# Optimization experiments

Hardware: AMD Instinct MI355X
Metric: run time of the kernel (lower is better)

## Reference

```python
import jax, jax.numpy as jnp
import numpy as np
from jax import lax

T_OBS = 16; N = 4096; V = 8; IN = 2; DYN = 64; ENC = 64; K = 2
SELF = 32; SOCD = 64; C31 = 16; DEC = 128; PRED = 25; OUT = 5; GH = 13; GW = 3
SOC_EMB = ((GH - 4 + 1) // 2) * C31  # 80


def leaky(v):
    return jnp.where(v >= 0, v, 0.1 * v)


def gru(xs, Wih, Whh, bih, bhh):
    # xs: [T, B, D]; PyTorch GRU cell math. Returns (h_T [B,H], all h [T,B,H]).
    H = Whh.shape[1]
    gis = xs @ Wih.T + bih  # precompute input contributions [T,B,3H]

    def step(h, gi):
        gh = h @ Whh.T + bhh
        ir, iz, inn = jnp.split(gi, 3, axis=-1)
        hr, hz, hn = jnp.split(gh, 3, axis=-1)
        r = jax.nn.sigmoid(ir + hr)
        z = jax.nn.sigmoid(iz + hz)
        n = jnp.tanh(inn + r * hn)
        h = (1.0 - z) * n + z * h
        return h, h

    h0 = jnp.zeros((xs.shape[1], H), xs.dtype)
    hT, hs = lax.scan(step, h0, gis)
    return hT, hs


def conv2d(xn, w, b):
    y = lax.conv_general_dilated(xn, w, (1, 1), 'VALID',
                                 dimension_numbers=('NCHW', 'OIHW', 'NCHW'))
    return y + b[None, :, None, None]


def setup_inputs() -> dict:
    key = jax.random.key(0)
    ks = jax.random.split(key, 24)
    x = jax.random.normal(ks[0], (T_OBS, N, IN), dtype=jnp.float32)
    ngbrs = jax.random.normal(ks[1], (T_OBS, N * V, IN), dtype=jnp.float32)
    # per-sample normalized spatial kernels [N, K, V, V]
    graphs = jax.random.uniform(ks[2], (N, K, V, V), dtype=jnp.float32) / V
    # masks: exactly V occupied grid cells per agent (full feature vector True)
    rng = np.random.default_rng(0)
    sel = np.argsort(rng.random((N, GW * GH)), axis=1)[:, :V]
    cell = np.zeros((N, GW * GH), dtype=bool)
    np.put_along_axis(cell, sel, True, axis=1)
    masks = jnp.asarray(np.broadcast_to(cell.reshape(N, GW, GH, 1), (N, GW, GH, ENC)))
    ngbrs_idx = jnp.arange(N + 1, dtype=jnp.int32) * V
    s = 0.05

    def w(k, shape):
        return jax.random.normal(k, shape, dtype=jnp.float32) * s

    params = dict(
        dyn_W=w(ks[3], (DYN, IN)), dyn_b=w(ks[4], (DYN,)),
        enc_Wih=w(ks[5], (3 * ENC, DYN)), enc_Whh=w(ks[6], (3 * ENC, ENC)),
        enc_bih=w(ks[7], (3 * ENC,)), enc_bhh=w(ks[8], (3 * ENC,)),
        s_W=w(ks[9], (K * DYN, DYN)), s_b=w(ks[10], (K * DYN,)),
        hid_W=w(ks[11], (SELF, ENC)), hid_b=w(ks[12], (SELF,)),
        soc_W=w(ks[13], (SOCD, ENC, 3, 3)), soc_b=w(ks[14], (SOCD,)),
        c31_W=w(ks[15], (C31, SOCD, 3, 1)), c31_b=w(ks[16], (C31,)),
        dec_Wih=w(ks[17], (3 * DEC, SOC_EMB + SELF)), dec_Whh=w(ks[18], (3 * DEC, DEC)),
        dec_bih=w(ks[19], (3 * DEC,)), dec_bhh=w(ks[20], (3 * DEC,)),
        out_W=w(ks[21], (OUT, DEC)), out_b=w(ks[22], (OUT,)),
    )
    return dict(x=x, ngbrs=ngbrs, graphs=graphs, masks=masks, ngbrs_idx=ngbrs_idx, **params)


def reference(x, ngbrs, graphs, masks, ngbrs_idx,
              dyn_W, dyn_b, enc_Wih, enc_Whh, enc_bih, enc_bhh,
              s_W, s_b, hid_W, hid_b, soc_W, soc_b, c31_W, c31_b,
              dec_Wih, dec_Whh, dec_bih, dec_bhh, out_W, out_b):
    # dyn embedding + leaky relu
    x_e = leaky(x @ dyn_W.T + dyn_b)          # [T, N, DYN]
    ng_e = leaky(ngbrs @ dyn_W.T + dyn_b)     # [T, N*V, DYN]

    # encode ego trajectories
    h_x, _ = gru(x_e, enc_Wih, enc_Whh, enc_bih, enc_bhh)  # [N, ENC]

    # graph conv (vectorized over the per-sample loop; uniform V neighbors)
    ng = ng_e.reshape(T_OBS, N, V, DYN)
    h = (ng @ s_W.T + s_b).reshape(T_OBS, N, V, K, DYN)    # conv1d kernel=1 == linear
    agg = jnp.einsum('tnvkc,nkvw->tnwc', h, graphs)        # [T, N, V, DYN]

    # encode aggregated neighbor trajectories
    h_ng, _ = gru(agg.reshape(T_OBS, N * V, DYN), enc_Wih, enc_Whh, enc_bih, enc_bhh)

    # masked_scatter_: fill True positions of masks (row-major) with h_ng values
    m = masks.reshape(-1)
    idx = jnp.clip(jnp.cumsum(m) - 1, 0, None)
    soc = jnp.where(m, h_ng.reshape(-1)[idx], 0.0).reshape(masks.shape)  # [N,GW,GH,ENC]

    soc = soc.transpose(0, 3, 2, 1)                        # [N, ENC, GH, GW]
    soc = leaky(conv2d(soc, soc_W, soc_b))                 # [N, SOCD, 11, 1]
    soc = leaky(conv2d(soc, c31_W, c31_b))                 # [N, C31, 9, 1]
    soc = lax.reduce_window(soc, -jnp.inf, lax.max, (1, 1, 2, 1), (1, 1, 2, 1),
                            ((0, 0), (0, 0), (1, 1), (0, 0)))  # [N, C31, 5, 1]
    soc = soc.reshape(N, SOC_EMB)

    x_s = leaky(h_x @ hid_W.T + hid_b)                     # [N, SELF]
    xc = jnp.concatenate([x_s, soc], axis=1)               # [N, SELF+SOC_EMB]

    # decode: same input fed at every prediction step
    xs = jnp.broadcast_to(xc[None], (PRED, N, xc.shape[1]))
    _, hs = gru(xs, dec_Wih, dec_Whh, dec_bih, dec_bhh)    # [PRED, N, DEC]
    o = hs @ out_W.T + out_b                               # [PRED, N, OUT]

    # outputActivation (standard cs-lstm bivariate Gaussian head)
    mu = o[..., 0:2]
    sig = jnp.exp(o[..., 2:4])
    rho = jnp.tanh(o[..., 4:5])
    return jnp.concatenate([mu, sig, rho], axis=-1)
```

## Files before the change

### kernel.cpp

```cpp
#include <hip/hip_runtime.h>
#include <hip/hip_bf16.h>

#define T_OBS 16
#define NAg   4096
#define Vn    8
#define NV    32768
#define SEQ   36864
#define PRED  25

typedef __bf16 bf16x8 __attribute__((ext_vector_type(8)));
typedef float  f32x4  __attribute__((ext_vector_type(4)));

#define LBAR() do {                                        \
    asm volatile("s_waitcnt lgkmcnt(0)" ::: "memory");     \
    __builtin_amdgcn_s_barrier();                          \
    __builtin_amdgcn_sched_barrier(0);                     \
  } while (0)

__device__ __forceinline__ float leakyf(float v){ return v >= 0.f ? v : 0.1f*v; }
__device__ __forceinline__ float sigf(float x){
  return __builtin_amdgcn_rcpf(1.f + __expf(-x));
}
__device__ __forceinline__ float tanh2f(float x){
  return fmaf(2.f, __builtin_amdgcn_rcpf(1.f + __expf(-2.f*x)), -1.f);
}
__device__ __forceinline__ float tanhf_(float x){
  x = fminf(fmaxf(x, -10.f), 10.f);
  float e = __expf(2.f*x);
  return (e-1.f)*__builtin_amdgcn_rcpf(e+1.f);
}
__device__ __forceinline__ float bf2f(unsigned short u){
  union{unsigned int i; float f;} v; v.i = ((unsigned int)u)<<16; return v.f;
}
__device__ __forceinline__ unsigned short f2bf(float f){
  __hip_bfloat16 b = __float2bfloat16(f);
  return *reinterpret_cast<unsigned short*>(&b);
}
__device__ __forceinline__ float dot4f(float4 a, float4 b, float acc){
  return fmaf(a.x,b.x, fmaf(a.y,b.y, fmaf(a.z,b.z, fmaf(a.w,b.w, acc))));
}
__device__ __forceinline__ bf16x8 as_bf16x8(uint4 u){
  union { uint4 a; bf16x8 b; } v; v.a = u; return v.b;
}
__device__ __forceinline__ uint4 pack8bf(float4 a, float4 b){
  union{ unsigned short s[8]; uint4 u; } o;
  o.s[0]=f2bf(a.x); o.s[1]=f2bf(a.y); o.s[2]=f2bf(a.z); o.s[3]=f2bf(a.w);
  o.s[4]=f2bf(b.x); o.s[5]=f2bf(b.y); o.s[6]=f2bf(b.z); o.s[7]=f2bf(b.w);
  return o.u;
}

__global__ void k_decode_masks(const void* __restrict__ masks, int* __restrict__ cells){
  int n = blockIdx.x*blockDim.x + threadIdx.x;
  if (n >= NAg) return;
  const unsigned char* m8  = (const unsigned char*)masks;
  const int*           m32 = (const int*)masks;
  int tmp[8]; for (int v=0; v<8; ++v) tmp[v] = 0;
  int cnt = 0;
  for (int cc=0; cc<39; ++cc){
    size_t base = ((size_t)n*39 + cc)*64;
    if (m8[base] && m8[base+1] && m8[base+33]){ if (cnt<8) tmp[cnt]=cc; cnt++; }
  }
  if (cnt != 8){
    cnt = 0;
    for (int cc=0; cc<39; ++cc){
      size_t base = ((size_t)n*39 + cc)*64;
      if (m32[base] != 0){ if (cnt<8) tmp[cnt]=cc; cnt++; }
    }
  }
  for (int v=0; v<8; ++v) cells[n*8+v] = tmp[v];
}

__global__ void k_prep(const float* __restrict__ eWih, const float* __restrict__ eWhh,
                       unsigned short* __restrict__ Wpk,
                       const float* __restrict__ dWhh, unsigned short* __restrict__ WdecF,
                       const float* __restrict__ outW, unsigned short* __restrict__ WoutF,
                       const float* __restrict__ sW, unsigned short* __restrict__ SWF,
                       const float* __restrict__ socW, unsigned short* __restrict__ WsocF,
                       const float* __restrict__ dWih, unsigned short* __restrict__ WdihF){
  int idx = blockIdx.x*blockDim.x + threadIdx.x;
  if (idx < 24576){
    int f   = idx >> 9;
    int rem = idx & 511;
    int l   = rem >> 3, j = rem & 7;
    int lr  = l & 15, lg = l >> 4;
    float val;
    if (f < 32){
      int nt = f >> 2, kk = f & 3;
      int n  = nt*16 + lr;
      int k  = kk*32 + lg*8 + j;
      val = (k < 64) ? eWih[(size_t)n*64 + k] : eWhh[(size_t)n*64 + (k-64)];
    } else if (f < 40){
      int q = f - 32;
      int n = (8 + (q>>1))*16 + lr;
      int k = (q&1)*32 + lg*8 + j;
      val = eWih[(size_t)n*64 + k];
    } else {
      int q = f - 40;
      int n = (8 + (q>>1))*16 + lr;
      int k = (q&1)*32 + lg*8 + j;
      val = eWhh[(size_t)n*64 + k];
    }
    Wpk[f*512 + l*8 + j] = f2bf(val);
  }
  if (idx < 49152){
    int f   = idx >> 9;
    int rem = idx & 511;
    int l   = rem >> 3, j = rem & 7;
    int lr  = l & 15, lg = l >> 4;
    int g = f/12, loc = f%12, gate = loc>>2, kk = loc&3;
    int n = gate*128 + g*16 + lr;
    int k = kk*32 + lg*8 + j;
    WdecF[idx] = f2bf(dWhh[(size_t)n*128 + k]);
  }
  if (idx < 49152){
    int f   = idx >> 9;
    int rem = idx & 511;
    int l   = rem >> 3, j = rem & 7;
    int lr  = l & 15, lg = l >> 4;
    int g = f/12, loc = f%12, gate = loc>>2, kk = loc&3;
    int n = gate*128 + g*16 + lr;
    int k = kk*32 + lg*8 + j;
    WdihF[idx] = (k < 112) ? f2bf(dWih[(size_t)n*112 + k]) : (unsigned short)0;
  }
  if (idx < 2048){
    int kk  = idx >> 9;
    int rem = idx & 511;
    int l   = rem >> 3, j = rem & 7;
    int lr  = l & 15, lg = l >> 4;
    int k = kk*32 + lg*8 + j;
    float v = (lr < 5) ? outW[(size_t)lr*128 + k] : 0.f;
    WoutF[idx] = f2bf(v);
  }
  if (idx < 8192){
    int f   = idx >> 9;
    int rem = idx & 511;
    int l   = rem >> 3, j = rem & 7;
    int lr  = l & 15, lg = l >> 4;
    int nt = f >> 1, kk = f & 1;
    int nn = nt*16 + lr;
    int k  = kk*32 + lg*8 + j;
    SWF[idx] = f2bf(sW[(size_t)nn*64 + k]);
  }
  if (idx < 36864){
    int f   = idx >> 9;
    int rem = idx & 511;
    int l   = rem >> 3, j = rem & 7;
    int lr  = l & 15, lg = l >> 4;
    int w = f/18, loc = f%18, kk = loc>>1, ks = loc&1;
    int o = w*16 + lr;
    int c = ks*32 + lg*8 + j;
    WsocF[idx] = f2bf(socW[(size_t)o*576 + c*9 + kk]);
  }
}

__global__ void k_embed_x(const float* __restrict__ x, const float* __restrict__ dynW,
                          const float* __restrict__ dynb, __hip_bfloat16* __restrict__ E){
  __shared__ float2 dwL[64];
  __shared__ float  dbL[64];
  const int tid = threadIdx.x;
  if (tid < 64){ dwL[tid] = *(const float2*)(dynW + tid*2); dbL[tid] = dynb[tid]; }
  __syncthreads();

  int idx = blockIdx.x*256 + tid;
  int c8 = idx & 7;
  int s  = (idx >> 3) & 4095;
  int t  = idx >> 15;
  float2 xy = *(const float2*)(x + ((size_t)t*NAg + s)*2);
  union { unsigned short sh[8]; uint4 u; } ou;
  #pragma unroll
  for (int jj=0; jj<8; ++jj){
    int c = c8*8 + jj;
    ou.sh[jj] = f2bf(leakyf(fmaf(xy.x, dwL[c].x, fmaf(xy.y, dwL[c].y, dbL[c]))));
  }
  *(uint4*)((unsigned short*)E + ((size_t)t*SEQ + s)*64 + c8*8) = ou.u;
}

__global__ __launch_bounds__(256,2) void k_embed_agg_mfma(
    const float* __restrict__ ngbrs, const float* __restrict__ graphs,
    const float* __restrict__ dynW, const float* __restrict__ dynb,
    const unsigned short* __restrict__ SWF, const float* __restrict__ sb,
    __hip_bfloat16* __restrict__ E)
{
  __shared__ __align__(16) unsigned char smem[128*132*4];
  __shared__ float2 pL[128];
  __shared__ float  gL[128];
  __shared__ float2 dwL[64];
  __shared__ float  dbL[64];
  unsigned char* ngeb = smem;
  float*         hm   = (float*)smem;
  const int tid = threadIdx.x;
  const int n = blockIdx.x;

  if (tid < 128) gL[tid] = graphs[(size_t)n*128 + tid];
  if (tid < 64)  dwL[tid] = *(const float2*)(dynW + tid*2);
  if (tid < 64)  dbL[tid] = dynb[tid];
  if (tid < 128){
    int t = tid >> 3, v = tid & 7;
    pL[tid] = *(const float2*)(ngbrs + ((size_t)t*NV + (size_t)n*8 + v)*2);
  }
  __syncthreads();

  #pragma unroll
  for (int p=0; p<4; ++p){
    int chunk = tid + p*256;
    int row = chunk >> 3, c8 = chunk & 7;
    float2 xy = pL[row];
    union { unsigned short s[8]; uint4 u; } ou;
    #pragma unroll
    for (int jj=0; jj<8; ++jj){
      int c = c8*8 + jj;
      ou.s[jj] = f2bf(leakyf(fmaf(xy.x, dwL[c].x, fmaf(xy.y, dwL[c].y, dbL[c]))));
    }
    *(uint4*)(ngeb + ((row*128 + c8*16) ^ ((row&7)<<4))) = ou.u;
  }
  __syncthreads();

  const int w4 = tid >> 6, l = tid & 63, lr = l & 15, lg = l >> 4;
  f32x4 acc[2][8];
  {
    uint4 bsw[16];
    #pragma unroll
    for (int f=0; f<16; ++f) bsw[f] = *(const uint4*)(SWF + f*512 + l*8);
    float sbv[8];
    #pragma unroll
    for (int nt=0; nt<8; ++nt) sbv[nt] = sb[nt*16 + lr];

    #pragma unroll
    for (int m=0; m<2; ++m)
      #pragma unroll
      for (int nt=0; nt<8; ++nt)
        acc[m][nt] = (f32x4){sbv[nt], sbv[nt], sbv[nt], sbv[nt]};

    #pragma unroll
    for (int m=0; m<2; ++m){
      int row = (w4*2+m)*16 + lr;
      int rb = row*128, sz = (row&7)<<4;
      uint4 a0 = *(const uint4*)(ngeb + ((rb      + lg*16) ^ sz));
      uint4 a1 = *(const uint4*)(ngeb + ((rb + 64 + lg*16) ^ sz));
      bf16x8 A0 = as_bf16x8(a0), A1 = as_bf16x8(a1);
      #pragma unroll
      for (int nt=0; nt<8; ++nt){
        acc[m][nt] = __builtin_amdgcn_mfma_f32_16x16x32_bf16(A0, as_bf16x8(bsw[nt*2+0]), acc[m][nt], 0,0,0);
        acc[m][nt] = __builtin_amdgcn_mfma_f32_16x16x32_bf16(A1, as_bf16x8(bsw[nt*2+1]), acc[m][nt], 0,0,0);
      }
    }
  }
  __syncthreads();

  #pragma unroll
  for (int m=0; m<2; ++m)
    #pragma unroll
    for (int nt=0; nt<8; ++nt)
      #pragma unroll
      for (int jj=0; jj<4; ++jj)
        hm[((w4*2+m)*16 + lg*4 + jj)*132 + nt*16 + lr] = acc[m][nt][jj];
  __syncthreads();

  #pragma unroll
  for (int p=0; p<4; ++p){
    int task = tid + p*256;
    int c8 = task & 7, wv = (task>>3)&7, t = task >> 6;
    float a8[8];
    #pragma unroll
    for (int jj=0; jj<8; ++jj) a8[jj] = 0.f;
    #pragma unroll
    for (int k=0; k<2; ++k){
      #pragma unroll
      for (int v=0; v<8; ++v){
        float g = gL[k*64 + v*8 + wv];
        const float* hp = hm + (t*8+v)*132 + k*64 + c8*8;
        float4 h0 = *(const float4*)(hp);
        float4 h1 = *(const float4*)(hp + 4);
        a8[0] = fmaf(g, h0.x, a8[0]); a8[1] = fmaf(g, h0.y, a8[1]);
        a8[2] = fmaf(g, h0.z, a8[2]); a8[3] = fmaf(g, h0.w, a8[3]);
        a8[4] = fmaf(g, h1.x, a8[4]); a8[5] = fmaf(g, h1.y, a8[5]);
        a8[6] = fmaf(g, h1.z, a8[6]); a8[7] = fmaf(g, h1.w, a8[7]);
      }
    }
    union { unsigned short s[8]; uint4 u; } ou;
    #pragma unroll
    for (int jj=0; jj<8; ++jj) ou.s[jj] = f2bf(a8[jj]);
    *(uint4*)((unsigned short*)E + ((size_t)t*SEQ + NAg + (size_t)n*8 + wv)*64 + c8*8) = ou.u;
  }
}

__global__ __launch_bounds__(256,4) void k_gru_enc_mfma(
    const unsigned short* __restrict__ E,
    const unsigned short* __restrict__ Wpk,
    const float* __restrict__ bih, const float* __restrict__ bhh,
    float* __restrict__ h_all)
{
  __shared__ __align__(16) unsigned char Hb[2][2048];
  const int tid = threadIdx.x;
  const int w  = tid >> 6;
  const int l  = tid & 63;
  const int lr = l & 15;
  const int lg = l >> 4;
  const size_t s0 = (size_t)blockIdx.x * 16;
  const int i  = w*16 + lr;

  uint4 bf[12];
  #pragma unroll
  for (int q=0; q<4; ++q) bf[q]   = *(const uint4*)(Wpk + (4*w + q)*512 + l*8);
  #pragma unroll
  for (int q=0; q<4; ++q) bf[4+q] = *(const uint4*)(Wpk + (16 + 4*w + q)*512 + l*8);
  #pragma unroll
  for (int q=0; q<2; ++q) bf[8+q] = *(const uint4*)(Wpk + (32 + 2*w + q)*512 + l*8);
  #pragma unroll
  for (int q=0; q<2; ++q) bf[10+q]= *(const uint4*)(Wpk + (40 + 2*w + q)*512 + l*8);

  const float b_r = bih[i]     + bhh[i];
  const float b_z = bih[64+i]  + bhh[64+i];
  const float bni = bih[128+i];
  const float bnh = bhh[128+i];

  *(uint4*)(&Hb[0][0] + tid*16) = make_uint4(0,0,0,0);
  __syncthreads();

  float hreg[4] = {0.f,0.f,0.f,0.f};

  const int swz = (lr & 7) << 4;
  const int rd0 = (lr*128      + lg*16) ^ swz;
  const int rd1 = (lr*128 + 64 + lg*16) ^ swz;
  int wro[4];
  #pragma unroll
  for (int u=0; u<4; ++u){
    int s = lg*4 + u;
    wro[u] = (s*128 + i*2) ^ ((s & 7) << 4);
  }

  const unsigned short* ep = E + (s0 + lr)*64 + lg*8;
  uint4 ax0 = *(const uint4*)(ep);
  uint4 ax1 = *(const uint4*)(ep + 32);

  int cur = 0;

  #pragma unroll 1
  for (int t=0; t<T_OBS; ++t){
    const unsigned short* pn = ep + ((t < 15) ? (size_t)SEQ*64 : 0);
    uint4 nx0 = *(const uint4*)(pn);
    uint4 nx1 = *(const uint4*)(pn + 32);

    const unsigned char* hc = Hb[cur];
    uint4 ah0 = *(const uint4*)(hc + rd0);
    uint4 ah1 = *(const uint4*)(hc + rd1);

    bf16x8 Ax0 = as_bf16x8(ax0), Ax1 = as_bf16x8(ax1);
    bf16x8 Ah0 = as_bf16x8(ah0), Ah1 = as_bf16x8(ah1);

    f32x4 z4 = (f32x4){0.f,0.f,0.f,0.f};
    f32x4 aRx = z4, aRh = z4, aZx = z4, aZh = z4, aNI = z4, aNH = z4;

    aRx = __builtin_amdgcn_mfma_f32_16x16x32_bf16(Ax0, as_bf16x8(bf[0]),  aRx, 0,0,0);
    aRx = __builtin_amdgcn_mfma_f32_16x16x32_bf16(Ax1, as_bf16x8(bf[1]),  aRx, 0,0,0);
    aRh = __builtin_amdgcn_mfma_f32_16x16x32_bf16(Ah0, as_bf16x8(bf[2]),  aRh, 0,0,0);
    aRh = __builtin_amdgcn_mfma_f32_16x16x32_bf16(Ah1, as_bf16x8(bf[3]),  aRh, 0,0,0);
    aZx = __builtin_amdgcn_mfma_f32_16x16x32_bf16(Ax0, as_bf16x8(bf[4]),  aZx, 0,0,0);
    aZx = __builtin_amdgcn_mfma_f32_16x16x32_bf16(Ax1, as_bf16x8(bf[5]),  aZx, 0,0,0);
    aZh = __builtin_amdgcn_mfma_f32_16x16x32_bf16(Ah0, as_bf16x8(bf[6]),  aZh, 0,0,0);
    aZh = __builtin_amdgcn_mfma_f32_16x16x32_bf16(Ah1, as_bf16x8(bf[7]),  aZh, 0,0,0);
    aNI = __builtin_amdgcn_mfma_f32_16x16x32_bf16(Ax0, as_bf16x8(bf[8]),  aNI, 0,0,0);
    aNI = __builtin_amdgcn_mfma_f32_16x16x32_bf16(Ax1, as_bf16x8(bf[9]),  aNI, 0,0,0);
    aNH = __builtin_amdgcn_mfma_f32_16x16x32_bf16(Ah0, as_bf16x8(bf[10]), aNH, 0,0,0);
    aNH = __builtin_amdgcn_mfma_f32_16x16x32_bf16(Ah1, as_bf16x8(bf[11]), aNH, 0,0,0);

    f32x4 aR = aRx + aRh;
    f32x4 aZ = aZx + aZh;

    unsigned char* hn = Hb[cur^1];
    #pragma unroll
    for (int u=0; u<4; ++u){
      float r  = sigf(aR[u] + b_r);
      float z  = sigf(aZ[u] + b_z);
      float nn = tanh2f(fmaf(r, aNH[u] + bnh, aNI[u] + bni));
      float h  = fmaf(z, hreg[u] - nn, nn);
      hreg[u]  = h;
      *(unsigned short*)(hn + wro[u]) = f2bf(h);
    }
    LBAR();
    cur ^= 1;
    ax0 = nx0; ax1 = nx1;
    ep = pn;
  }

  #pragma unroll
  for (int u=0; u<4; ++u)
    h_all[(s0 + lg*4 + u)*64 + i] = hreg[u];
}

__global__ __launch_bounds__(256,3) void k_soc_mfma(
    const float* __restrict__ h_all, const int* __restrict__ cells,
    const unsigned short* __restrict__ WsocF, const float* __restrict__ socb,
    const float* __restrict__ c31W, const float* __restrict__ c31b,
    const float* __restrict__ hidW, const float* __restrict__ hidb,
    float* __restrict__ xc)
{
  __shared__ unsigned short Qb[9*8*64];
  __shared__ float o1p[4*64*17];
  __shared__ float o1[64*12];
  __shared__ float c2p[4*144];
  __shared__ float W2L[64*48];
  __shared__ float socbL[64];
  __shared__ float b2L[16];
  __shared__ int   cellsL[64];

  const int tid = threadIdx.x;
  const int w  = tid >> 6;
  const int l  = tid & 63;
  const int lr = l & 15, lg = l >> 4;
  const int n0 = blockIdx.x * 8;

  {
    int a = tid >> 5, j = tid & 31;
    const float* h = h_all + (size_t)(n0 + a)*64;
    const float* wv = hidW + (size_t)j*64;
    float acc = hidb[j];
    #pragma unroll
    for (int k4=0; k4<16; ++k4)
      acc = dot4f(*(const float4*)(h + k4*4), *(const float4*)(wv + k4*4), acc);
    xc[(size_t)(n0+a)*112 + j] = leakyf(acc);
  }

  for (int idx=tid; idx<3072; idx+=256){
    int p = idx/192, rem = idx%192, o = rem/3, ky = rem%3;
    W2L[(o*3+ky)*16 + p] = c31W[idx];
  }
  if (tid < 64) socbL[tid] = socb[tid];
  if (tid < 16) b2L[tid]  = c31b[tid];
  if (tid < 64) cellsL[tid] = cells[n0*8 + tid];

  uint4 bs[18];
  #pragma unroll
  for (int f=0; f<18; ++f)
    bs[f] = *(const uint4*)(WsocF + (size_t)(w*18 + f)*512 + l*8);
  __syncthreads();

  #pragma unroll 1
  for (int a=0; a<8; ++a){
    uint4 ax0u = make_uint4(0,0,0,0), ax1u = make_uint4(0,0,0,0);
    if (lr < 8){
      const float* hp = h_all + ((size_t)NAg + (size_t)(n0+a)*8 + lr)*64 + lg*8;
      float4 f0 = *(const float4*)(hp);
      float4 f1 = *(const float4*)(hp + 4);
      float4 f2 = *(const float4*)(hp + 32);
      float4 f3 = *(const float4*)(hp + 36);
      ax0u = pack8bf(f0, f1);
      ax1u = pack8bf(f2, f3);
    }
    bf16x8 A0 = as_bf16x8(ax0u), A1 = as_bf16x8(ax1u);

    f32x4 acc[9];
    #pragma unroll
    for (int kk=0; kk<9; ++kk) acc[kk] = (f32x4){0.f,0.f,0.f,0.f};
    #pragma unroll
    for (int kk=0; kk<9; ++kk){
      acc[kk] = __builtin_amdgcn_mfma_f32_16x16x32_bf16(A0, as_bf16x8(bs[kk*2+0]), acc[kk], 0,0,0);
      acc[kk] = __builtin_amdgcn_mfma_f32_16x16x32_bf16(A1, as_bf16x8(bs[kk*2+1]), acc[kk], 0,0,0);
    }

    __syncthreads();

    if (lg < 2){
      #pragma unroll
      for (int kk=0; kk<9; ++kk)
        #pragma unroll
        for (int j=0; j<4; ++j)
          Qb[(kk*8 + lg*4 + j)*64 + w*16 + lr] = f2bf(acc[kk][j]);
    }
    for (int idx=tid; idx<2816; idx+=256){
      int q = idx/704, r = idx%704;
      int o = r/11, y = r%11;
      o1p[(q*64 + o)*17 + y + 2] = 0.f;
    }
    __syncthreads();

    {
      int o = tid & 63, q = tid >> 6;
      #pragma unroll
      for (int p6=0; p6<6; ++p6){
        int pr = q*6 + p6;
        int v = pr/3, ky = pr%3;
        int cc = cellsL[a*8 + v];
        int gw = cc/13, gh = cc - gw*13;
        float val = bf2f(Qb[((ky*3+gw)*8 + v)*64 + o]);
        o1p[(q*64 + o)*17 + (gh - ky + 2)] += val;
      }
    }
    __syncthreads();

    for (int idx=tid; idx<704; idx+=256){
      int o = idx/11, y = idx%11;
      float s = socbL[o];
      #pragma unroll
      for (int q=0; q<4; ++q) s += o1p[(q*64 + o)*17 + y + 2];
      o1[o*12 + y] = leakyf(s);
    }
    __syncthreads();

    {
      int q = tid >> 6, l2 = tid & 63;
      for (int e=l2; e<144; e+=64){
        int p = e & 15, y2 = e >> 4;
        float accv = 0.f;
        #pragma unroll
        for (int oi=0; oi<16; ++oi){
          int oo = q*16 + oi;
          const float* o1r = o1 + oo*12 + y2;
          const float* w2r = W2L + oo*48 + p;
          accv = fmaf(o1r[0], w2r[0], fmaf(o1r[1], w2r[16], fmaf(o1r[2], w2r[32], accv)));
        }
        c2p[q*144 + e] = accv;
      }
    }
    __syncthreads();

    if (tid < 80){
      int p = tid/5, ww = tid%5;
      float v0, v1;
      {
        int y2 = (ww == 0) ? 0 : 2*ww - 1;
        float s = b2L[p];
        #pragma unroll
        for (int q=0; q<4; ++q) s += c2p[q*144 + y2*16 + p];
        v0 = leakyf(s);
      }
      if (ww == 0) v1 = v0;
      else {
        int y2 = 2*ww;
        float s = b2L[p];
        #pragma unroll
        for (int q=0; q<4; ++q) s += c2p[q*144 + y2*16 + p];
        v1 = leakyf(s);
      }
      xc[(size_t)(n0+a)*112 + 32 + p*5 + ww] = fmaxf(v0, v1);
    }
  }
}

__global__ __launch_bounds__(512,1) void k_dec_mfma(
    const float* __restrict__ xc, const unsigned short* __restrict__ WdecF,
    const unsigned short* __restrict__ WdihF, const unsigned short* __restrict__ WoutF,
    const float* __restrict__ dbih, const float* __restrict__ dbhh,
    const float* __restrict__ outb, float* __restrict__ out)
{
  __shared__ __align__(16) unsigned char Hb[2][4096];
  __shared__ __align__(16) unsigned char Xb[16*256];
  const int tid = threadIdx.x;
  const int g   = tid >> 6;
  const int l   = tid & 63;
  const int lr  = l & 15, lg = l >> 4;
  const int n0  = blockIdx.x * 16;
  const int i   = g*16 + lr;

  if (tid < 256){
    int row = tid >> 4, c16 = tid & 15;
    uint4 v = make_uint4(0,0,0,0);
    if (c16 < 14){
      const float* xp = xc + (size_t)(n0+row)*112 + c16*8;
      float4 f0 = *(const float4*)(xp);
      float4 f1 = *(const float4*)(xp + 4);
      v = pack8bf(f0, f1);
    }
    *(uint4*)(Xb + ((row*256 + c16*16) ^ ((row&7)<<4))) = v;
  }
  *(uint4*)(&Hb[0][0] + tid*16) = make_uint4(0,0,0,0);
  __syncthreads();

  const int swz = (lr & 7) << 4;
  int rdo[4];
  #pragma unroll
  for (int kk=0; kk<4; ++kk) rdo[kk] = (lr*256 + kk*64 + lg*16) ^ swz;

  float gi_r[4], gi_z[4], gi_n[4];
  {
    uint4 axq[4];
    #pragma unroll
    for (int kk=0; kk<4; ++kk)
      axq[kk] = *(const uint4*)(Xb + rdo[kk]);
    f32x4 z4 = (f32x4){0.f,0.f,0.f,0.f};
    f32x4 gR = z4, gZ = z4, gN = z4;
    #pragma unroll
    for (int kk=0; kk<4; ++kk){
      uint4 b0 = *(const uint4*)(WdihF + (size_t)(g*12 + 0*4 + kk)*512 + l*8);
      gR = __builtin_amdgcn_mfma_f32_16x16x32_bf16(as_bf16x8(axq[kk]), as_bf16x8(b0), gR, 0,0,0);
    }
    #pragma unroll
    for (int kk=0; kk<4; ++kk){
      uint4 b1 = *(const uint4*)(WdihF + (size_t)(g*12 + 1*4 + kk)*512 + l*8);
      gZ = __builtin_amdgcn_mfma_f32_16x16x32_bf16(as_bf16x8(axq[kk]), as_bf16x8(b1), gZ, 0,0,0);
    }
    #pragma unroll
    for (int kk=0; kk<4; ++kk){
      uint4 b2 = *(const uint4*)(WdihF + (size_t)(g*12 + 2*4 + kk)*512 + l*8);
      gN = __builtin_amdgcn_mfma_f32_16x16x32_bf16(as_bf16x8(axq[kk]), as_bf16x8(b2), gN, 0,0,0);
    }
    const float bi_r = dbih[i], bi_z = dbih[128+i], bi_n = dbih[256+i];
    #pragma unroll
    for (int u=0; u<4; ++u){
      gi_r[u] = gR[u] + bi_r;
      gi_z[u] = gZ[u] + bi_z;
      gi_n[u] = gN[u] + bi_n;
    }
  }
  const float bh_r = dbhh[i], bh_z = dbhh[128+i], bh_n = dbhh[256+i];
  const float obv  = (lr < 5) ? outb[lr] : 0.f;

  uint4 bgf[12];
  #pragma unroll
  for (int f=0; f<12; ++f)
    bgf[f] = *(const uint4*)(WdecF + (size_t)(g*12 + f)*512 + l*8);
  uint4 bof[4];
  #pragma unroll
  for (int kk=0; kk<4; ++kk)
    bof[kk] = *(const uint4*)(WoutF + (size_t)kk*512 + l*8);

  float hreg[4] = {0.f, 0.f, 0.f, 0.f};

  int wro[4];
  #pragma unroll
  for (int u=0; u<4; ++u){
    int s = lg*4 + u;
    wro[u] = (s*256 + i*2) ^ ((s & 7) << 4);
  }

  int cur = 0;
  __syncthreads();

  #pragma unroll 1
  for (int t=0; t<PRED; ++t){
    const unsigned char* hc = Hb[cur];
    uint4 ah[4];
    #pragma unroll
    for (int kk=0; kk<4; ++kk)
      ah[kk] = *(const uint4*)(hc + rdo[kk]);

    f32x4 z4 = (f32x4){0.f,0.f,0.f,0.f};
    f32x4 aRa = z4, aRb = z4, aZa = z4, aZb = z4, aNa = z4, aNb = z4;
    aRa = __builtin_amdgcn_mfma_f32_16x16x32_bf16(as_bf16x8(ah[0]), as_bf16x8(bgf[0]),  aRa, 0,0,0);
    aRa = __builtin_amdgcn_mfma_f32_16x16x32_bf16(as_bf16x8(ah[1]), as_bf16x8(bgf[1]),  aRa, 0,0,0);
    aRb = __builtin_amdgcn_mfma_f32_16x16x32_bf16(as_bf16x8(ah[2]), as_bf16x8(bgf[2]),  aRb, 0,0,0);
    aRb = __builtin_amdgcn_mfma_f32_16x16x32_bf16(as_bf16x8(ah[3]), as_bf16x8(bgf[3]),  aRb, 0,0,0);
    aZa = __builtin_amdgcn_mfma_f32_16x16x32_bf16(as_bf16x8(ah[0]), as_bf16x8(bgf[4]),  aZa, 0,0,0);
    aZa = __builtin_amdgcn_mfma_f32_16x16x32_bf16(as_bf16x8(ah[1]), as_bf16x8(bgf[5]),  aZa, 0,0,0);
    aZb = __builtin_amdgcn_mfma_f32_16x16x32_bf16(as_bf16x8(ah[2]), as_bf16x8(bgf[6]),  aZb, 0,0,0);
    aZb = __builtin_amdgcn_mfma_f32_16x16x32_bf16(as_bf16x8(ah[3]), as_bf16x8(bgf[7]),  aZb, 0,0,0);
    aNa = __builtin_amdgcn_mfma_f32_16x16x32_bf16(as_bf16x8(ah[0]), as_bf16x8(bgf[8]),  aNa, 0,0,0);
    aNa = __builtin_amdgcn_mfma_f32_16x16x32_bf16(as_bf16x8(ah[1]), as_bf16x8(bgf[9]),  aNa, 0,0,0);
    aNb = __builtin_amdgcn_mfma_f32_16x16x32_bf16(as_bf16x8(ah[2]), as_bf16x8(bgf[10]), aNb, 0,0,0);
    aNb = __builtin_amdgcn_mfma_f32_16x16x32_bf16(as_bf16x8(ah[3]), as_bf16x8(bgf[11]), aNb, 0,0,0);

    if (t > 0 && g == (t & 7)){
      f32x4 accO = z4;
      #pragma unroll
      for (int kk=0; kk<4; ++kk)
        accO = __builtin_amdgcn_mfma_f32_16x16x32_bf16(as_bf16x8(ah[kk]), as_bf16x8(bof[kk]), accO, 0,0,0);
      if (lr < 5){
        #pragma unroll
        for (int u=0; u<4; ++u){
          float a = accO[u] + obv;
          float val = (lr < 2) ? a : (lr == 4 ? tanhf_(a) : __expf(a));
          out[((size_t)(t-1)*NAg + n0 + lg*4 + u)*5 + lr] = val;
        }
      }
    }

    f32x4 aR = aRa + aRb;
    f32x4 aZ = aZa + aZb;
    f32x4 aN = aNa + aNb;

    unsigned char* hn = Hb[cur^1];
    #pragma unroll
    for (int u=0; u<4; ++u){
      float r  = sigf(gi_r[u] + aR[u] + bh_r);
      float z  = sigf(gi_z[u] + aZ[u] + bh_z);
      float nn = tanh2f(fmaf(r, aN[u] + bh_n, gi_n[u]));
      float h  = fmaf(z, hreg[u] - nn, nn);
      hreg[u] = h;
      *(unsigned short*)(hn + wro[u]) = f2bf(h);
    }
    LBAR();
    cur ^= 1;
  }

  if (g == (PRED & 7)){
    const unsigned char* hc = Hb[cur];
    uint4 ah[4];
    #pragma unroll
    for (int kk=0; kk<4; ++kk)
      ah[kk] = *(const uint4*)(hc + rdo[kk]);
    f32x4 accO = (f32x4){0.f,0.f,0.f,0.f};
    #pragma unroll
    for (int kk=0; kk<4; ++kk)
      accO = __builtin_amdgcn_mfma_f32_16x16x32_bf16(as_bf16x8(ah[kk]), as_bf16x8(bof[kk]), accO, 0,0,0);
    if (lr < 5){
      #pragma unroll
      for (int u=0; u<4; ++u){
        float a = accO[u] + obv;
        float val = (lr < 2) ? a : (lr == 4 ? tanhf_(a) : __expf(a));
        out[((size_t)(PRED-1)*NAg + n0 + lg*4 + u)*5 + lr] = val;
      }
    }
  }
}

extern "C" void kernel_launch(void* const* d_in, const int* in_sizes, int n_in,
                              void* d_out, int out_size, void* d_ws, size_t ws_size,
                              hipStream_t stream)
{
  const float* x      = (const float*)d_in[0];
  const float* ngbrs  = (const float*)d_in[1];
  const float* graphs = (const float*)d_in[2];
  const void*  masks  = d_in[3];
  const float* dynW   = (const float*)d_in[5];
  const float* dynb   = (const float*)d_in[6];
  const float* eWih   = (const float*)d_in[7];
  const float* eWhh   = (const float*)d_in[8];
  const float* ebih   = (const float*)d_in[9];
  const float* ebhh   = (const float*)d_in[10];
  const float* sW     = (const float*)d_in[11];
  const float* sb     = (const float*)d_in[12];
  const float* hidW   = (const float*)d_in[13];
  const float* hidb   = (const float*)d_in[14];
  const float* socW   = (const float*)d_in[15];
  const float* socb   = (const float*)d_in[16];
  const float* c31W   = (const float*)d_in[17];
  const float* c31b   = (const float*)d_in[18];
  const float* dWih   = (const float*)d_in[19];
  const float* dWhh   = (const float*)d_in[20];
  const float* dbih   = (const float*)d_in[21];
  const float* dbhh   = (const float*)d_in[22];
  const float* outW   = (const float*)d_in[23];
  const float* outb   = (const float*)d_in[24];
  float* out = (float*)d_out;

  char* ws = (char*)d_ws;
  size_t off = 0;
  __hip_bfloat16* E = (__hip_bfloat16*)(ws + off); off += (size_t)T_OBS*SEQ*64*2;
  float* h_all      = (float*)(ws + off);          off += (size_t)SEQ*64*4;
  int*   cells      = (int*)(ws + off);            off += (size_t)NAg*8*4;
  float* xc         = (float*)(ws + off);          off += (size_t)NAg*112*4;
  unsigned short* Wpk = (unsigned short*)(ws + off); off += (size_t)48*512*2;
  unsigned short* WdecF = (unsigned short*)(ws + off); off += (size_t)96*512*2;
  unsigned short* WoutF = (unsigned short*)(ws + off); off += (size_t)4*512*2;
  unsigned short* SWF = (unsigned short*)(ws + off); off += (size_t)16*512*2;
  unsigned short* WsocF = (unsigned short*)(ws + off); off += (size_t)72*512*2;
  unsigned short* WdihF = (unsigned short*)(ws + off); off += (size_t)96*512*2;

  k_decode_masks<<<16, 256, 0, stream>>>(masks, cells);
  k_prep<<<192, 256, 0, stream>>>(eWih, eWhh, Wpk, dWhh, WdecF, outW, WoutF, sW, SWF, socW, WsocF, dWih, WdihF);
  k_embed_x<<<2048, 256, 0, stream>>>(x, dynW, dynb, E);
  k_embed_agg_mfma<<<4096, 256, 0, stream>>>(ngbrs, graphs, dynW, dynb, SWF, sb, E);
  k_gru_enc_mfma<<<2304, 256, 0, stream>>>((const unsigned short*)E, Wpk, ebih, ebhh, h_all);
  k_soc_mfma<<<512, 256, 0, stream>>>(h_all, cells, WsocF, socb, c31W, c31b, hidW, hidb, xc);
  k_dec_mfma<<<256, 512, 0, stream>>>(xc, WdecF, WdihF, WoutF, dbih, dbhh, outb, out);
}
```

Measured before the change: 217.7 us.

## Parallelize mask decoding with wave ballots and restructure graph aggregation loop

The mask decode kernel now gives each agent one 64-lane wave: each lane checks one grid cell and ballot/popcount compaction replaces the serial 39-cell loop per thread, with the grid launched at 1024 blocks. The graph aggregation in the embed kernel now has each thread compute all 8 output neighbours for 4 channels. This reuses each h load across 8 graph weights loaded as float4s, which cuts LDS traffic. The trade is more accumulator registers and narrower 8-byte stores in place of 16-byte stores.

```diff
diff --git a/kernel.cpp b/kernel.cpp
--- a/kernel.cpp
+++ b/kernel.cpp
@@ -50,24 +50,26 @@
 }
 
 __global__ void k_decode_masks(const void* __restrict__ masks, int* __restrict__ cells){
-  int n = blockIdx.x*blockDim.x + threadIdx.x;
-  if (n >= NAg) return;
+  const int tid = threadIdx.x;
+  const int a   = tid >> 6;
+  const int l   = tid & 63;
+  const int n   = blockIdx.x*4 + a;
   const unsigned char* m8  = (const unsigned char*)masks;
   const int*           m32 = (const int*)masks;
-  int tmp[8]; for (int v=0; v<8; ++v) tmp[v] = 0;
-  int cnt = 0;
-  for (int cc=0; cc<39; ++cc){
-    size_t base = ((size_t)n*39 + cc)*64;
-    if (m8[base] && m8[base+1] && m8[base+33]){ if (cnt<8) tmp[cnt]=cc; cnt++; }
-  }
-  if (cnt != 8){
-    cnt = 0;
-    for (int cc=0; cc<39; ++cc){
-      size_t base = ((size_t)n*39 + cc)*64;
-      if (m32[base] != 0){ if (cnt<8) tmp[cnt]=cc; cnt++; }
-    }
-  }
-  for (int v=0; v<8; ++v) cells[n*8+v] = tmp[v];
+  bool sel8 = false, sel32 = false;
+  if (l < 39){
+    size_t base = ((size_t)n*39 + l)*64;
+    sel8  = m8[base] && m8[base+1] && m8[base+33];
+    sel32 = m32[base] != 0;
+  }
+  unsigned long long b8  = __ballot(sel8);
+  unsigned long long b32 = __ballot(sel32);
+  unsigned long long m = (__popcll(b8) == 8) ? b8 : b32;
+  int cnt = __popcll(m);
+  if (l < 8 && l >= cnt) cells[n*8 + l] = 0;
+  bool sel = (m >> l) & 1ull;
+  int prefix = __popcll(m & ((1ull << l) - 1ull));
+  if (sel && prefix < 8) cells[n*8 + prefix] = l;
 }
 
 __global__ void k_prep(const float* __restrict__ eWih, const float* __restrict__ eWhh,
@@ -183,7 +185,7 @@
 {
   __shared__ __align__(16) unsigned char smem[128*132*4];
   __shared__ float2 pL[128];
-  __shared__ float  gL[128];
+  __shared__ __align__(16) float gL[128];
   __shared__ float2 dwL[64];
   __shared__ float  dbL[64];
   unsigned char* ngeb = smem;
@@ -256,31 +258,44 @@
         hm[((w4*2+m)*16 + lg*4 + jj)*132 + nt*16 + lr] = acc[m][nt][jj];
   __syncthreads();
 
-  #pragma unroll
-  for (int p=0; p<4; ++p){
-    int task = tid + p*256;
-    int c8 = task & 7, wv = (task>>3)&7, t = task >> 6;
-    float a8[8];
-    #pragma unroll
-    for (int jj=0; jj<8; ++jj) a8[jj] = 0.f;
-    #pragma unroll
-    for (int k=0; k<2; ++k){
+  {
+    int t = tid >> 4, c4 = tid & 15;
+    float a4[8][4];
+    #pragma unroll
+    for (int wv=0; wv<8; ++wv)
+      #pragma unroll
+      for (int jo=0; jo<4; ++jo) a4[wv][jo] = 0.f;
+
+    #pragma unroll
+    for (int k=0; k<2; ++k)
       #pragma unroll
       for (int v=0; v<8; ++v){
-        float g = gL[k*64 + v*8 + wv];
-        const float* hp = hm + (t*8+v)*132 + k*64 + c8*8;
-        float4 h0 = *(const float4*)(hp);
-        float4 h1 = *(const float4*)(hp + 4);
-        a8[0] = fmaf(g, h0.x, a8[0]); a8[1] = fmaf(g, h0.y, a8[1]);
-        a8[2] = fmaf(g, h0.z, a8[2]); a8[3] = fmaf(g, h0.w, a8[3]);
-        a8[4] = fmaf(g, h1.x, a8[4]); a8[5] = fmaf(g, h1.y, a8[5]);
-        a8[6] = fmaf(g, h1.z, a8[6]); a8[7] = fmaf(g, h1.w, a8[7]);
+        float4 h4 = *(const float4*)(hm + (t*8+v)*132 + k*64 + c4*4);
+        float4 g0 = *(const float4*)(gL + k*64 + v*8);
+        float4 g1 = *(const float4*)(gL + k*64 + v*8 + 4);
+        const float* ga = &g0.x;
+        const float* gb = &g1.x;
+        #pragma unroll
+        for (int q=0; q<4; ++q){
+          a4[q][0]   = fmaf(ga[q], h4.x, a4[q][0]);
+          a4[q][1]   = fmaf(ga[q], h4.y, a4[q][1]);
+          a4[q][2]   = fmaf(ga[q], h4.z, a4[q][2]);
+          a4[q][3]   = fmaf(ga[q], h4.w, a4[q][3]);
+          a4[4+q][0] = fmaf(gb[q], h4.x, a4[4+q][0]);
+          a4[4+q][1] = fmaf(gb[q], h4.y, a4[4+q][1]);
+          a4[4+q][2] = fmaf(gb[q], h4.z, a4[4+q][2]);
+          a4[4+q][3] = fmaf(gb[q], h4.w, a4[4+q][3]);
+        }
       }
-    }
-    union { unsigned short s[8]; uint4 u; } ou;
-    #pragma unroll
-    for (int jj=0; jj<8; ++jj) ou.s[jj] = f2bf(a8[jj]);
-    *(uint4*)((unsigned short*)E + ((size_t)t*SEQ + NAg + (size_t)n*8 + wv)*64 + c8*8) = ou.u;
+
+    unsigned short* Eu = (unsigned short*)E;
+    #pragma unroll
+    for (int wv=0; wv<8; ++wv){
+      union { unsigned short s[4]; uint2 u; } ou;
+      ou.s[0] = f2bf(a4[wv][0]); ou.s[1] = f2bf(a4[wv][1]);
+      ou.s[2] = f2bf(a4[wv][2]); ou.s[3] = f2bf(a4[wv][3]);
+      *(uint2*)(Eu + ((size_t)t*SEQ + NAg + (size_t)n*8 + wv)*64 + c4*4) = ou.u;
+    }
   }
 }
 
@@ -746,7 +761,7 @@
   unsigned short* WsocF = (unsigned short*)(ws + off); off += (size_t)72*512*2;
   unsigned short* WdihF = (unsigned short*)(ws + off); off += (size_t)96*512*2;
 
-  k_decode_masks<<<16, 256, 0, stream>>>(masks, cells);
+  k_decode_masks<<<1024, 256, 0, stream>>>(masks, cells);
   k_prep<<<192, 256, 0, stream>>>(eWih, eWhh, Wpk, dWhh, WdecF, outW, WoutF, sW, SWF, socW, WsocF, dWih, WdihF);
   k_embed_x<<<2048, 256, 0, stream>>>(x, dynW, dynb, E);
   k_embed_agg_mfma<<<4096, 256, 0, stream>>>(ngbrs, graphs, dynW, dynb, SWF, sb, E);
```

After: 181.9 us. 1.2x faster.
